# Optimization experiments

Measured on AMD Instinct MI355X. Metric: run time of the kernel, lower is better.

The kernel has to match this reference:

```python
import jax, jax.numpy as jnp
import numpy as np

B, L, D = 8, 2048, 64

def setup_inputs() -> dict:
    key = jax.random.key(0)
    k1, k2 = jax.random.split(key)
    query = jax.random.normal(k1, (B, L, D), dtype=jnp.float32)
    key_t = jax.random.normal(k2, (B, L, D), dtype=jnp.float32)
    return {"query": query, "key": key_t}

def reference(query, key):
    d = query.shape[-1]
    # scores: [B, Lq, Lk] = Q K^T / sqrt(d)
    scores = jnp.einsum('bqd,bkd->bqk', query, key) / jnp.sqrt(jnp.asarray(d, query.dtype))
    weights = jax.nn.softmax(scores, axis=-1)  # dropout p=0.0 -> identity
    # output uses `key` as values, matching the original module
    return jnp.einsum('bqk,bkd->bqd', weights, key)
```

## Files before the change

kernel.cpp:

```cpp
#include <hip/hip_runtime.h>


#define LL 2048
#define DD 64
#define BQ 128
#define BK 64
#define KPAD 72
#define NSEG 8
#define NQB (LL / BQ)

typedef __attribute__((ext_vector_type(8))) short bf16x8;
typedef __attribute__((ext_vector_type(4))) float f32x4;
typedef __attribute__((ext_vector_type(16))) float f32x16;
typedef __attribute__((ext_vector_type(4))) unsigned short u16x4;
typedef __attribute__((ext_vector_type(2))) unsigned int u32x2;
typedef __attribute__((ext_vector_type(4))) unsigned int u32x4;

static __device__ __forceinline__ unsigned short f2bf(float f) {
  unsigned u = __builtin_bit_cast(unsigned, f);
  u += 0x7fffu + ((u >> 16) & 1u);
  return (unsigned short)(u >> 16);
}
static __device__ __forceinline__ float bf2f(unsigned short h) {
  unsigned u = (unsigned)h << 16;
  return __builtin_bit_cast(float, u);
}
static __device__ __forceinline__ unsigned cvtpk(float lo, float hi) {
  unsigned d;
  asm("v_cvt_pk_bf16_f32 %0, %1, %2" : "=v"(d) : "v"(lo), "v"(hi));
  return d;
}
#define PLSWAP(a, b) \
  asm volatile("v_permlane32_swap_b32 %0, %1" : "+v"(a), "+v"(b))

static __device__ __forceinline__ f32x16 zero16() {
  f32x16 z;
#pragma unroll
  for (int i = 0; i < 16; ++i) z[i] = 0.f;
  return z;
}

static __device__ __forceinline__ void exp_pack(const f32x16 sv, float& lp,
                                                bf16x8& o0, bf16x8& o1) {
  unsigned w[8];
#pragma unroll
  for (int m = 0; m < 8; ++m) {
    float pA = __builtin_amdgcn_exp2f(sv[2 * m]);
    float pB = __builtin_amdgcn_exp2f(sv[2 * m + 1]);
    lp += pA + pB;
    w[m] = cvtpk(pA, pB);
  }
  PLSWAP(w[0], w[2]);
  PLSWAP(w[1], w[3]);
  PLSWAP(w[4], w[6]);
  PLSWAP(w[5], w[7]);
  u32x4 lo = {w[0], w[1], w[2], w[3]};
  u32x4 hh = {w[4], w[5], w[6], w[7]};
  o0 = __builtin_bit_cast(bf16x8, lo);
  o1 = __builtin_bit_cast(bf16x8, hh);
}

__global__ __launch_bounds__(256, 4) void attn_kernel(
    const float* __restrict__ Q, const float* __restrict__ K,
    float* __restrict__ O, u16x4* __restrict__ Opart,
    float* __restrict__ Lp, int seglen, int nseg) {
  __shared__ __attribute__((aligned(16))) unsigned short sKt[2][BK][KPAD];
  __shared__ __attribute__((aligned(16))) unsigned short sKtT[2][DD * KPAD];

  const int tid  = threadIdx.x;
  const int wave = tid >> 6;
  const int lane = tid & 63;
  const int l31  = lane & 31;
  const int hi   = lane >> 5;

  const int batch = blockIdx.y;
  const int seg   = blockIdx.z;
  const int q0w   = blockIdx.x * BQ + wave * 32;
  const int ngroups = gridDim.y * NQB;
  const int gq    = batch * NQB + blockIdx.x;

  const float qs = 0.125f * 1.44269504f;
  bf16x8 bq[4];
  {
    const float* qrow = Q + (size_t)(batch * LL + q0w + l31) * DD;
#pragma unroll
    for (int dc = 0; dc < 4; ++dc) {
      const float* p = qrow + dc * 16 + hi * 8;
      float4 f0 = *(const float4*)(p);
      float4 f1 = *(const float4*)(p + 4);
      u32x4 d;
      d[0] = cvtpk(f0.x * qs, f0.y * qs);
      d[1] = cvtpk(f0.z * qs, f0.w * qs);
      d[2] = cvtpk(f1.x * qs, f1.y * qs);
      d[3] = cvtpk(f1.z * qs, f1.w * qs);
      bq[dc] = __builtin_bit_cast(bf16x8, d);
    }
  }

  f32x16 oacc[2];
  oacc[0] = zero16();
  oacc[1] = zero16();
  float l_a = 0.f, l_b = 0.f;

  const int niter = seglen / BK;
  const float* kbase = K + (size_t)(batch * LL + seg * seglen) * DD;
  const int kv_o  = tid >> 3;
  const int oc_o  = tid & 7;
  const int kv_o2 = kv_o + 32;

  float4 pf[2][2];
#pragma unroll
  for (int i = 0; i < 2; ++i) {
    int p = tid + i * 256;
    const float4* src = (const float4*)(kbase + (size_t)(p >> 3) * DD + (p & 7) * 8);
    pf[i][0] = src[0];
    pf[i][1] = src[1];
  }
#pragma unroll
  for (int i = 0; i < 2; ++i) {
    int kv = i ? kv_o2 : kv_o, oc = oc_o;
    u32x4 dw;
    dw[0] = cvtpk(pf[i][0].x, pf[i][0].y);
    dw[1] = cvtpk(pf[i][0].z, pf[i][0].w);
    dw[2] = cvtpk(pf[i][1].x, pf[i][1].y);
    dw[3] = cvtpk(pf[i][1].z, pf[i][1].w);
    *(u32x4*)&sKt[0][kv][oc * 8] = dw;
    int swz = ((kv >> 3) ^ oc) & 7;
    unsigned short* dst = &sKtT[0][(oc * 8) * KPAD + swz * 8 + (kv & 7)];
#pragma unroll
    for (int u = 0; u < 4; ++u) {
      dst[(2 * u) * KPAD]     = (unsigned short)dw[u];
      dst[(2 * u + 1) * KPAD] = (unsigned short)(dw[u] >> 16);
    }
  }
  __syncthreads();

  for (int t = 0; t < niter; ++t) {
    const int cur = t & 1;
    const int nxt = cur ^ 1;

    if (t + 1 < niter) {
      const float* kt = kbase + (size_t)(t + 1) * BK * DD;
#pragma unroll
      for (int i = 0; i < 2; ++i) {
        int p = tid + i * 256;
        const float4* src = (const float4*)(kt + (size_t)(p >> 3) * DD + (p & 7) * 8);
        pf[i][0] = src[0];
        pf[i][1] = src[1];
      }
    }

    bf16x8 pa[2][2];
    {
      f32x16 s0 = zero16();
#pragma unroll
      for (int dc = 0; dc < 4; ++dc) {
        bf16x8 a0 = *(const bf16x8*)&sKt[cur][l31][dc * 16 + hi * 8];
        s0 = __builtin_amdgcn_mfma_f32_32x32x16_bf16(a0, bq[dc], s0, 0, 0, 0);
      }
      exp_pack(s0, l_a, pa[0][0], pa[0][1]);
    }
    {
      f32x16 s1 = zero16();
#pragma unroll
      for (int dc = 0; dc < 4; ++dc) {
        bf16x8 a1 = *(const bf16x8*)&sKt[cur][32 + l31][dc * 16 + hi * 8];
        s1 = __builtin_amdgcn_mfma_f32_32x32x16_bf16(a1, bq[dc], s1, 0, 0, 0);
      }
      exp_pack(s1, l_b, pa[1][0], pa[1][1]);
    }

    if (t + 1 < niter) {
#pragma unroll
      for (int i = 0; i < 2; ++i) {
        int kv = i ? kv_o2 : kv_o, oc = oc_o;
        u32x4 dw;
        dw[0] = cvtpk(pf[i][0].x, pf[i][0].y);
        dw[1] = cvtpk(pf[i][0].z, pf[i][0].w);
        dw[2] = cvtpk(pf[i][1].x, pf[i][1].y);
        dw[3] = cvtpk(pf[i][1].z, pf[i][1].w);
        *(u32x4*)&sKt[nxt][kv][oc * 8] = dw;
        int swz = ((kv >> 3) ^ oc) & 7;
        unsigned short* dst = &sKtT[nxt][(oc * 8) * KPAD + swz * 8 + (kv & 7)];
#pragma unroll
        for (int u = 0; u < 4; ++u) {
          dst[(2 * u) * KPAD]     = (unsigned short)dw[u];
          dst[(2 * u + 1) * KPAD] = (unsigned short)(dw[u] >> 16);
        }
      }
    }

#pragma unroll
    for (int kk = 0; kk < 4; ++kk)
#pragma unroll
      for (int dt = 0; dt < 2; ++dt) {
        const int d = dt * 32 + l31;
        bf16x8 b = *(const bf16x8*)
            &sKtT[cur][d * KPAD + (((2 * kk + hi) ^ (d >> 3)) & 7) * 8];
        oacc[dt] = __builtin_amdgcn_mfma_f32_32x32x16_bf16(
            pa[kk >> 1][kk & 1], b, oacc[dt], 0, 0, 0);
      }

    __syncthreads();
  }

  float lt = l_a + l_b;
  lt += __shfl_xor(lt, 32);

  if (nseg == 1) {
#pragma unroll
    for (int dt = 0; dt < 2; ++dt)
#pragma unroll
      for (int g = 0; g < 4; ++g)
#pragma unroll
        for (int c = 0; c < 4; ++c) {
          const int q = 8 * g + 4 * hi + c;
          float lr = __shfl(lt, q, 64);
          O[(size_t)(batch * LL + q0w + q) * DD + dt * 32 + l31] =
              oacc[dt][4 * g + c] / lr;
        }
    return;
  }

  const size_t slotbase = ((size_t)seg * ngroups + gq) * 32 + wave * 8;
#pragma unroll
  for (int dt = 0; dt < 2; ++dt)
#pragma unroll
    for (int g = 0; g < 4; ++g) {
      u32x2 dw;
      dw[0] = cvtpk(oacc[dt][4 * g], oacc[dt][4 * g + 1]);
      dw[1] = cvtpk(oacc[dt][4 * g + 2], oacc[dt][4 * g + 3]);
      Opart[(slotbase + dt * 4 + g) * 64 + lane] = __builtin_bit_cast(u16x4, dw);
    }
  if (lane < 32)
    Lp[(((size_t)seg * ngroups + gq) * 4 + wave) * 32 + lane] = lt;
}

__global__ __launch_bounds__(256) void combine_kernel(
    const u16x4* __restrict__ Opart, const float* __restrict__ Lp,
    float* __restrict__ O, int nseg, int ngroups) {
  const int tid  = threadIdx.x;
  const int g    = blockIdx.x;
  const int slot = blockIdx.y * 4 + (tid >> 6);
  const int lane = tid & 63;
  const int l31  = lane & 31;
  const int hi   = lane >> 5;
  const int wv = slot >> 3, dt = (slot >> 2) & 1, rg = slot & 3;

  f32x4 acc = (f32x4){0.f, 0.f, 0.f, 0.f};
  f32x4 den = (f32x4){0.f, 0.f, 0.f, 0.f};
  for (int s = 0; s < nseg; ++s) {
    u16x4 h = Opart[((size_t)(s * ngroups + g) * 32 + slot) * 64 + lane];
    acc[0] += bf2f(h[0]); acc[1] += bf2f(h[1]);
    acc[2] += bf2f(h[2]); acc[3] += bf2f(h[3]);
    float4 d4 = *(const float4*)
        &Lp[(((size_t)s * ngroups + g) * 4 + wv) * 32 + 8 * rg + 4 * hi];
    den[0] += d4.x; den[1] += d4.y; den[2] += d4.z; den[3] += d4.w;
  }
  const int batch = g / NQB, qbx = g % NQB;
  const int rowbase = batch * LL + qbx * BQ + wv * 32 + 8 * rg + 4 * hi;
#pragma unroll
  for (int c = 0; c < 4; ++c)
    O[(size_t)(rowbase + c) * DD + dt * 32 + l31] = acc[c] / den[c];
}

extern "C" void kernel_launch(void* const* d_in, const int* in_sizes, int n_in,
                              void* d_out, int out_size, void* d_ws, size_t ws_size,
                              hipStream_t stream) {
  const float* Q = (const float*)d_in[0];
  const float* K = (const float*)d_in[1];
  float* O = (float*)d_out;
  int B = in_sizes[0] / (LL * DD);
  int ngroups = B * NQB;

  size_t opart_bytes = (size_t)NSEG * ngroups * 32 * 64 * sizeof(u16x4);
  size_t lp_bytes    = (size_t)NSEG * ngroups * 4 * 32 * sizeof(float);
  if (ws_size >= opart_bytes + lp_bytes) {
    u16x4* Opart = (u16x4*)d_ws;
    float* Lpp = (float*)((char*)d_ws + opart_bytes);
    dim3 grid(NQB, B, NSEG);
    attn_kernel<<<grid, 256, 0, stream>>>(Q, K, O, Opart, Lpp, LL / NSEG, NSEG);
    combine_kernel<<<dim3(ngroups, 8), 256, 0, stream>>>(Opart, Lpp, O, NSEG, ngroups);
  } else {
    dim3 grid(NQB, B, 1);
    attn_kernel<<<grid, 256, 0, stream>>>(Q, K, O, nullptr, nullptr, LL, 1);
  }
}
```

Measured before the change: 92.35 us.

## Software-pipeline PV of previous tile with QK of next using triple buffering

The K-tile loop is restructured into a three-stage software pipeline with triple-buffered LDS tiles. Each iteration runs the PV MFMAs for the previous tile together with the QK MFMAs for the current tile at raised wave priority, then does exp/pack while staging the next tile. Interleaving the two QK MFMA chains and splitting across fewer segments (NSEG 8 to 4) with launch bounds cut to 3 waves per SIMD trade occupancy and LDS for better matrix-core overlap and less partial-reduction work. The larger LDS footprint and lower occupancy may reduce latency hiding.

```diff
diff --git a/kernel.cpp b/kernel.cpp
--- a/kernel.cpp
+++ b/kernel.cpp
@@ -6,7 +6,7 @@
 #define BQ 128
 #define BK 64
 #define KPAD 72
-#define NSEG 8
+#define NSEG 4
 #define NQB (LL / BQ)
 
 typedef __attribute__((ext_vector_type(8))) short bf16x8;
@@ -60,12 +60,12 @@
   o1 = __builtin_bit_cast(bf16x8, hh);
 }
 
-__global__ __launch_bounds__(256, 4) void attn_kernel(
+__global__ __launch_bounds__(256, 3) void attn_kernel(
     const float* __restrict__ Q, const float* __restrict__ K,
     float* __restrict__ O, u16x4* __restrict__ Opart,
     float* __restrict__ Lp, int seglen, int nseg) {
-  __shared__ __attribute__((aligned(16))) unsigned short sKt[2][BK][KPAD];
-  __shared__ __attribute__((aligned(16))) unsigned short sKtT[2][DD * KPAD];
+  __shared__ __attribute__((aligned(16))) unsigned short sKt[3][BK][KPAD];
+  __shared__ __attribute__((aligned(16))) unsigned short sKtT[3][DD * KPAD];
 
   const int tid  = threadIdx.x;
   const int wave = tid >> 6;
@@ -109,100 +109,97 @@
   const int kv_o2 = kv_o + 32;
 
   float4 pf[2][2];
-#pragma unroll
-  for (int i = 0; i < 2; ++i) {
-    int p = tid + i * 256;
-    const float4* src = (const float4*)(kbase + (size_t)(p >> 3) * DD + (p & 7) * 8);
-    pf[i][0] = src[0];
-    pf[i][1] = src[1];
-  }
-#pragma unroll
-  for (int i = 0; i < 2; ++i) {
-    int kv = i ? kv_o2 : kv_o, oc = oc_o;
-    u32x4 dw;
-    dw[0] = cvtpk(pf[i][0].x, pf[i][0].y);
-    dw[1] = cvtpk(pf[i][0].z, pf[i][0].w);
-    dw[2] = cvtpk(pf[i][1].x, pf[i][1].y);
-    dw[3] = cvtpk(pf[i][1].z, pf[i][1].w);
-    *(u32x4*)&sKt[0][kv][oc * 8] = dw;
-    int swz = ((kv >> 3) ^ oc) & 7;
-    unsigned short* dst = &sKtT[0][(oc * 8) * KPAD + swz * 8 + (kv & 7)];
-#pragma unroll
-    for (int u = 0; u < 4; ++u) {
-      dst[(2 * u) * KPAD]     = (unsigned short)dw[u];
-      dst[(2 * u + 1) * KPAD] = (unsigned short)(dw[u] >> 16);
-    }
-  }
-  __syncthreads();
-
-  for (int t = 0; t < niter; ++t) {
-    const int cur = t & 1;
-    const int nxt = cur ^ 1;
-
-    if (t + 1 < niter) {
-      const float* kt = kbase + (size_t)(t + 1) * BK * DD;
-#pragma unroll
-      for (int i = 0; i < 2; ++i) {
-        int p = tid + i * 256;
-        const float4* src = (const float4*)(kt + (size_t)(p >> 3) * DD + (p & 7) * 8);
-        pf[i][0] = src[0];
-        pf[i][1] = src[1];
+  bf16x8 pa[2][2];
+
+  auto loadpf = [&](int t) {
+    const float* kt = kbase + (size_t)t * BK * DD;
+#pragma unroll
+    for (int i = 0; i < 2; ++i) {
+      int p = tid + i * 256;
+      const float4* src = (const float4*)(kt + (size_t)(p >> 3) * DD + (p & 7) * 8);
+      pf[i][0] = src[0];
+      pf[i][1] = src[1];
+    }
+  };
+
+  auto stage = [&](int b) {
+#pragma unroll
+    for (int i = 0; i < 2; ++i) {
+      int kv = i ? kv_o2 : kv_o, oc = oc_o;
+      u32x4 dw;
+      dw[0] = cvtpk(pf[i][0].x, pf[i][0].y);
+      dw[1] = cvtpk(pf[i][0].z, pf[i][0].w);
+      dw[2] = cvtpk(pf[i][1].x, pf[i][1].y);
+      dw[3] = cvtpk(pf[i][1].z, pf[i][1].w);
+      *(u32x4*)&sKt[b][kv][oc * 8] = dw;
+      int swz = ((kv >> 3) ^ oc) & 7;
+      unsigned short* dst = &sKtT[b][(oc * 8) * KPAD + swz * 8 + (kv & 7)];
+#pragma unroll
+      for (int u = 0; u < 4; ++u) {
+        dst[(2 * u) * KPAD]     = (unsigned short)dw[u];
+        dst[(2 * u + 1) * KPAD] = (unsigned short)(dw[u] >> 16);
       }
     }
-
-    bf16x8 pa[2][2];
-    {
-      f32x16 s0 = zero16();
-#pragma unroll
-      for (int dc = 0; dc < 4; ++dc) {
-        bf16x8 a0 = *(const bf16x8*)&sKt[cur][l31][dc * 16 + hi * 8];
-        s0 = __builtin_amdgcn_mfma_f32_32x32x16_bf16(a0, bq[dc], s0, 0, 0, 0);
-      }
-      exp_pack(s0, l_a, pa[0][0], pa[0][1]);
-    }
-    {
-      f32x16 s1 = zero16();
-#pragma unroll
-      for (int dc = 0; dc < 4; ++dc) {
-        bf16x8 a1 = *(const bf16x8*)&sKt[cur][32 + l31][dc * 16 + hi * 8];
-        s1 = __builtin_amdgcn_mfma_f32_32x32x16_bf16(a1, bq[dc], s1, 0, 0, 0);
-      }
-      exp_pack(s1, l_b, pa[1][0], pa[1][1]);
-    }
-
-    if (t + 1 < niter) {
-#pragma unroll
-      for (int i = 0; i < 2; ++i) {
-        int kv = i ? kv_o2 : kv_o, oc = oc_o;
-        u32x4 dw;
-        dw[0] = cvtpk(pf[i][0].x, pf[i][0].y);
-        dw[1] = cvtpk(pf[i][0].z, pf[i][0].w);
-        dw[2] = cvtpk(pf[i][1].x, pf[i][1].y);
-        dw[3] = cvtpk(pf[i][1].z, pf[i][1].w);
-        *(u32x4*)&sKt[nxt][kv][oc * 8] = dw;
-        int swz = ((kv >> 3) ^ oc) & 7;
-        unsigned short* dst = &sKtT[nxt][(oc * 8) * KPAD + swz * 8 + (kv & 7)];
-#pragma unroll
-        for (int u = 0; u < 4; ++u) {
-          dst[(2 * u) * KPAD]     = (unsigned short)dw[u];
-          dst[(2 * u + 1) * KPAD] = (unsigned short)(dw[u] >> 16);
-        }
-      }
-    }
-
+  };
+
+  auto qk_mfma = [&](int b, f32x16& s0, f32x16& s1) {
+    s0 = zero16();
+    s1 = zero16();
+#pragma unroll
+    for (int dc = 0; dc < 4; ++dc) {
+      bf16x8 a0 = *(const bf16x8*)&sKt[b][l31][dc * 16 + hi * 8];
+      bf16x8 a1 = *(const bf16x8*)&sKt[b][32 + l31][dc * 16 + hi * 8];
+      s0 = __builtin_amdgcn_mfma_f32_32x32x16_bf16(a0, bq[dc], s0, 0, 0, 0);
+      s1 = __builtin_amdgcn_mfma_f32_32x32x16_bf16(a1, bq[dc], s1, 0, 0, 0);
+    }
+  };
+
+  auto pv = [&](int b) {
 #pragma unroll
     for (int kk = 0; kk < 4; ++kk)
 #pragma unroll
       for (int dt = 0; dt < 2; ++dt) {
         const int d = dt * 32 + l31;
-        bf16x8 b = *(const bf16x8*)
-            &sKtT[cur][d * KPAD + (((2 * kk + hi) ^ (d >> 3)) & 7) * 8];
+        bf16x8 bb = *(const bf16x8*)
+            &sKtT[b][d * KPAD + (((2 * kk + hi) ^ (d >> 3)) & 7) * 8];
         oacc[dt] = __builtin_amdgcn_mfma_f32_32x32x16_bf16(
-            pa[kk >> 1][kk & 1], b, oacc[dt], 0, 0, 0);
+            pa[kk >> 1][kk & 1], bb, oacc[dt], 0, 0, 0);
       }
-
+  };
+
+  loadpf(0);
+  stage(0);
+  if (niter > 1) loadpf(1);
+  __syncthreads();
+  {
+    f32x16 s0, s1;
+    qk_mfma(0, s0, s1);
+    exp_pack(s0, l_a, pa[0][0], pa[0][1]);
+    exp_pack(s1, l_b, pa[1][0], pa[1][1]);
+  }
+  if (niter > 1) {
+    stage(1);
     __syncthreads();
   }
+
+  int b_pv = 0, b_qk = 1, b_st = 2;
+  for (int t = 1; t < niter; ++t) {
+    if (t + 1 < niter) loadpf(t + 1);
+    __builtin_amdgcn_s_setprio(1);
+    pv(b_pv);
+    f32x16 s0, s1;
+    qk_mfma(b_qk, s0, s1);
+    __builtin_amdgcn_s_setprio(0);
+    exp_pack(s0, l_a, pa[0][0], pa[0][1]);
+    exp_pack(s1, l_b, pa[1][0], pa[1][1]);
+    if (t + 1 < niter) {
+      stage(b_st);
+      __syncthreads();
+    } else if (t + 1 == niter && niter > 1) {
+    }
+    int tmp = b_pv; b_pv = b_qk; b_qk = b_st; b_st = tmp;
+  }
+  pv(b_pv);
 
   float lt = l_a + l_b;
   lt += __shfl_xor(lt, 32);
```

After: 77.94 us. 15.6% less time.
